# Performance work log

Hardware: AMD Instinct MI355X
Metric: run time of the kernel (lower is better)

Reference implementation:

```python
import jax, jax.numpy as jnp
import numpy as np

H = 32        # attention heads
HKV = 32      # kv heads (MHA)
D = 128       # head size
HID = 4096    # hidden size
B = 4         # sequences in prefill batch
S = 1024      # tokens per sequence
T = B * S     # total tokens
NUM_BLOCKS = 64
BLOCK_SIZE = 128


def setup_inputs() -> dict:
    key = jax.random.key(0)
    ks = jax.random.split(key, 6)
    hidden_states = jax.random.normal(ks[0], (T, HID), jnp.float32) * 0.02
    theta = jax.random.uniform(ks[1], (T, D // 2), jnp.float32) * 6.2831853
    cos = jnp.cos(theta)
    sin = jnp.sin(theta)
    qkv_w = jax.random.normal(ks[2], (HID, (H + 2 * HKV) * D), jnp.float32) * (HID ** -0.5)
    o_w = jax.random.normal(ks[3], (H * D, HID), jnp.float32) * ((H * D) ** -0.5)
    key_cache = jnp.zeros((NUM_BLOCKS, BLOCK_SIZE, HKV, D), jnp.float32)
    value_cache = jnp.zeros((NUM_BLOCKS, BLOCK_SIZE, HKV, D), jnp.float32)
    cu_seqlen_prefill = jnp.arange(B + 1, dtype=jnp.int32) * S
    slots = jnp.arange(T, dtype=jnp.int32)
    block_tables = jnp.arange(B * (S // BLOCK_SIZE), dtype=jnp.int32).reshape(B, S // BLOCK_SIZE)
    input_lengths = jnp.full((B,), S, jnp.int32)
    return dict(hidden_states=hidden_states, cos=cos, sin=sin, qkv_w=qkv_w, o_w=o_w,
                key_cache=key_cache, value_cache=value_cache,
                cu_seqlen_prefill=cu_seqlen_prefill, slots=slots,
                block_tables=block_tables, input_lengths=input_lengths, max_s=S)


def _rope(x, cos, sin):
    # neox-style rotary: split head dim in half. x: [T, h, D], cos/sin: [T, D/2]
    d2 = x.shape[-1] // 2
    x1, x2 = x[..., :d2], x[..., d2:]
    c, s = cos[:, None, :], sin[:, None, :]
    return jnp.concatenate([x1 * c - x2 * s, x2 * c + x1 * s], axis=-1)


def reference(hidden_states, cos, sin, qkv_w, o_w, key_cache, value_cache,
              cu_seqlen_prefill, slots, block_tables, input_lengths, max_s):
    T_ = hidden_states.shape[0]
    B_ = input_lengths.shape[0]
    S_ = T_ // B_  # equal-length prefill sequences per cu_seqlen_prefill
    # fused QKV projection
    qkv = hidden_states @ qkv_w                      # [T, (H+2Hkv)*D]
    q = qkv[:, :H * D].reshape(T_, H, D)
    kv = qkv[:, H * D:].reshape(T_, 2, HKV, D)
    k, v = kv[:, 0], kv[:, 1]
    # rotary embedding on q and k (in-place in original)
    q = _rope(q, cos, sin)
    k = _rope(k, cos, sin)
    # reshape_and_cache: scatter rotated K / raw V into paged KV cache by flat slot
    kc = key_cache.reshape(-1, HKV, D).at[slots].set(k).reshape(key_cache.shape)
    vc = value_cache.reshape(-1, HKV, D).at[slots].set(v).reshape(value_cache.shape)
    # varlen causal flash attention (prefill branch); equal seqlens -> dense [B,S]
    scale = D ** -0.5
    qb = q.reshape(B_, S_, H, D)
    kb = k.reshape(B_, S_, HKV, D)
    vb = v.reshape(B_, S_, HKV, D)
    scores = jnp.einsum('bqhd,bkhd->bhqk', qb, kb) * scale   # [B,H,S,S]
    idx = jnp.arange(S_)
    causal = idx[:, None] >= idx[None, :]
    scores = jnp.where(causal[None, None], scores, jnp.finfo(scores.dtype).min)
    probs = jax.nn.softmax(scores, axis=-1)
    attn = jnp.einsum('bhqk,bkhd->bqhd', probs, vb).reshape(T_, H * D)
    out = attn @ o_w                                 # o_proj, no bias
    return out, kc, vc
```

## Files before the change

kernel.cpp:

```cpp
#include <hip/hip_runtime.h>

#define HQ 32
#define HKV 32
#define DH 128
#define HID 4096
#define BATCH 4
#define SEQ 1024
#define TOK (BATCH * SEQ)
#define NQKV 12288
#define CACHE_ROWS 8192
#define SM_SCALE 0.08838834764831845f

typedef unsigned short u16;
typedef __bf16 bf16x8 __attribute__((ext_vector_type(8)));
typedef float floatx4 __attribute__((ext_vector_type(4)));
typedef u16 u16x8 __attribute__((ext_vector_type(8)));
typedef u16 u16x4 __attribute__((ext_vector_type(4)));

__device__ __forceinline__ u16 f2bf(float x) {
  unsigned u = __float_as_uint(x);
  u += 0x7FFF + ((u >> 16) & 1);
  return (u16)(u >> 16);
}
__device__ __forceinline__ float bf2f(u16 h) {
  return __uint_as_float(((unsigned)h) << 16);
}
__device__ __forceinline__ void cp16(const void* g, void* l) {
  __builtin_amdgcn_global_load_lds(
      (__attribute__((address_space(1))) unsigned int*)(g),
      (__attribute__((address_space(3))) unsigned int*)(l), 16, 0, 0);
}

__global__ void k_f32_to_bf16(const float4* __restrict__ x, ushort4* __restrict__ y) {
  int i = blockIdx.x * 256 + threadIdx.x;
  float4 v = x[i];
  ushort4 o;
  o.x = f2bf(v.x); o.y = f2bf(v.y); o.z = f2bf(v.z); o.w = f2bf(v.w);
  y[i] = o;
}

__global__ void k_transpose_bf16(const float* __restrict__ W, u16* __restrict__ Wt,
                                 int Kd, int Nd) {
  __shared__ float t[64][65];
  int n0 = blockIdx.x << 6, k0 = blockIdx.y << 6;
  int tx = threadIdx.x & 63, ty = threadIdx.x >> 6;
#pragma unroll
  for (int r = ty; r < 64; r += 4)
    t[r][tx] = W[(size_t)(k0 + r) * Nd + n0 + tx];
  __syncthreads();
  const int kg = threadIdx.x & 15, nr = threadIdx.x >> 4;
#pragma unroll
  for (int q = 0; q < 4; ++q) {
    int n = q * 16 + nr;
    u16x4 o;
#pragma unroll
    for (int j = 0; j < 4; ++j) o[j] = f2bf(t[kg * 4 + j][n]);
    *(u16x4*)&Wt[(size_t)(n0 + n) * Kd + k0 + kg * 4] = o;
  }
}

template <int Nd, int Kd, bool OUT_BF16>
__global__ __launch_bounds__(512, 2) void k_gemm256(const u16* __restrict__ A,
                                                    const u16* __restrict__ Bt,
                                                    void* __restrict__ Cp) {
  constexpr int GX = Nd / 256;
  constexpr int NWG = (TOK / 256) * GX;
  constexpr int BAND = 4 * GX;
  __shared__ __align__(16) u16 lds[2][2][256 * 64];

  const int bid = blockIdx.x;
  const int j = (bid & 7) * (NWG / 8) + (bid >> 3);
  const int band = j / BAND, r = j % BAND;
  const int by = band * 4 + (r & 3), bx = r >> 2;
  const int bm = by << 8, bn = bx << 8;

  const int tid = threadIdx.x;
  const int wave = tid >> 6, lane = tid & 63;
  const int wm = wave >> 2, wn = wave & 3;
  const int quad = lane >> 4, l16 = lane & 15;

  auto stage_half = [&](const u16* src, int grow, int k0, u16* ldsb, int h) {
#pragma unroll
    for (int p = 0; p < 2; ++p) {
      int g = tid + (p << 9);
      int row = g >> 3, ps = g & 7;
      int ls = ps ^ (row & 7);
      cp16(src + (size_t)(grow + h * 128 + row) * Kd + k0 + ls * 8,
           ldsb + ((h * 128 + row) << 6) + (ps << 3));
    }
  };
  auto frag = [&](const u16* ldsb, int row, int slot) {
    return (const bf16x8*)(ldsb + (row << 6) + ((slot ^ (row & 7)) << 3));
  };

  const floatx4 FZ4 = {0.f, 0.f, 0.f, 0.f};
  floatx4 acc[8][4];
#pragma unroll
  for (int i = 0; i < 8; ++i)
#pragma unroll
    for (int j2 = 0; j2 < 4; ++j2) acc[i][j2] = FZ4;

  stage_half(A, bm, 0, &lds[0][0][0], 0);
  stage_half(A, bm, 0, &lds[0][0][0], 1);
  stage_half(Bt, bn, 0, &lds[0][1][0], 0);
  stage_half(Bt, bn, 0, &lds[0][1][0], 1);
  stage_half(Bt, bn, 64, &lds[1][1][0], 0);
  stage_half(Bt, bn, 64, &lds[1][1][0], 1);
  asm volatile("s_waitcnt vmcnt(4)" ::: "memory");
  asm volatile("s_barrier" ::: "memory");

  constexpr int NT = Kd / 64;
  for (int t = 0; t < NT; ++t) {
    const int c = t & 1, o = c ^ 1;
    const u16* cA = &lds[c][0][0];
    const u16* cB = &lds[c][1][0];
    const int k1 = (t + 1 < NT) ? (t + 1) * 64 : (Kd - 64);
    const int k2 = (t + 2 < NT) ? (t + 2) * 64 : (Kd - 64);

    bf16x8 bfr[4][2];
#pragma unroll
    for (int ph = 0; ph < 4; ++ph) {
      if (ph == 0) {
#pragma unroll
        for (int ni = 0; ni < 4; ++ni)
#pragma unroll
          for (int ks = 0; ks < 2; ++ks)
            bfr[ni][ks] = *frag(cB, wn * 64 + ni * 16 + l16, ks * 4 + quad);
      }
      bf16x8 af[2][2];
#pragma unroll
      for (int m = 0; m < 2; ++m)
#pragma unroll
        for (int ks = 0; ks < 2; ++ks)
          af[m][ks] = *frag(cA, wm * 128 + (ph * 2 + m) * 16 + l16, ks * 4 + quad);

      if (ph == 0) stage_half(A, bm, k1, &lds[o][0][0], 0);
      else if (ph == 1) stage_half(A, bm, k1, &lds[o][0][0], 1);
      else if (ph == 2) stage_half(Bt, bn, k2, &lds[c][1][0], 0);
      else stage_half(Bt, bn, k2, &lds[c][1][0], 1);

      asm volatile("s_barrier" ::: "memory");
      __builtin_amdgcn_s_setprio(1);
#pragma unroll
      for (int m = 0; m < 2; ++m)
#pragma unroll
        for (int ni = 0; ni < 4; ++ni)
#pragma unroll
          for (int ks = 0; ks < 2; ++ks)
            acc[ph * 2 + m][ni] = __builtin_amdgcn_mfma_f32_16x16x32_bf16(
                af[m][ks], bfr[ni][ks], acc[ph * 2 + m][ni], 0, 0, 0);
      __builtin_amdgcn_s_setprio(0);
      if (ph == 3) asm volatile("s_waitcnt vmcnt(4)" ::: "memory");
      asm volatile("s_barrier" ::: "memory");
    }
  }
  asm volatile("s_waitcnt vmcnt(0)" ::: "memory");

  const int rbase = bm + wm * 128 + quad * 4;
  const int cbase = bn + wn * 64 + l16;
#pragma unroll
  for (int mi = 0; mi < 8; ++mi)
#pragma unroll
    for (int ni = 0; ni < 4; ++ni)
#pragma unroll
      for (int r2 = 0; r2 < 4; ++r2) {
        size_t idx = (size_t)(rbase + mi * 16 + r2) * Nd + (cbase + ni * 16);
        if (OUT_BF16)
          ((u16*)Cp)[idx] = f2bf(acc[mi][ni][r2]);
        else
          ((float*)Cp)[idx] = acc[mi][ni][r2];
      }
}

__global__ void k_rope_scatter(const u16* __restrict__ qkv, const float* __restrict__ cosp,
                               const float* __restrict__ sinp, const int* __restrict__ slots,
                               u16* __restrict__ qb, u16* __restrict__ kb,
                               float* __restrict__ kc, float* __restrict__ vc) {
  const int t = blockIdx.x;
  const int b = t >> 10, s = t & 1023;
  const int tid = threadIdx.x;
  __shared__ float lc[64], ls[64];
  if (tid < 64) lc[tid] = cosp[t * 64 + tid];
  else if (tid < 128) ls[tid - 64] = sinp[t * 64 + (tid - 64)];
  __syncthreads();
  const int slot = slots[t];
  const u16* base = qkv + (size_t)t * NQKV;
  const int h = tid >> 3, i0 = (tid & 7) << 3;
  float c[8], sn[8];
#pragma unroll
  for (int j = 0; j < 8; ++j) { c[j] = lc[i0 + j]; sn[j] = ls[i0 + j]; }

  {
    u16x8 x1 = *(const u16x8*)&base[h * 128 + i0];
    u16x8 x2 = *(const u16x8*)&base[h * 128 + 64 + i0];
    u16x8 y1, y2;
#pragma unroll
    for (int j = 0; j < 8; ++j) {
      float a = bf2f(x1[j]), d = bf2f(x2[j]);
      y1[j] = f2bf((a * c[j] - d * sn[j]) * SM_SCALE);
      y2[j] = f2bf((d * c[j] + a * sn[j]) * SM_SCALE);
    }
    size_t o = ((size_t)(b * HQ + h) * SEQ + s) * DH + i0;
    *(u16x8*)&qb[o] = y1;
    *(u16x8*)&qb[o + 64] = y2;
  }
  {
    u16x8 x1 = *(const u16x8*)&base[HQ * DH + h * 128 + i0];
    u16x8 x2 = *(const u16x8*)&base[HQ * DH + h * 128 + 64 + i0];
    u16x8 y1, y2;
    float f1[8], f2[8];
#pragma unroll
    for (int j = 0; j < 8; ++j) {
      float a = bf2f(x1[j]), d = bf2f(x2[j]);
      f1[j] = a * c[j] - d * sn[j];
      f2[j] = d * c[j] + a * sn[j];
      y1[j] = f2bf(f1[j]);
      y2[j] = f2bf(f2[j]);
    }
    size_t o = ((size_t)(b * HKV + h) * SEQ + s) * DH + i0;
    *(u16x8*)&kb[o] = y1;
    *(u16x8*)&kb[o + 64] = y2;
    size_t oc = (size_t)slot * (HKV * DH) + h * 128 + i0;
    *(float4*)&kc[oc]      = make_float4(f1[0], f1[1], f1[2], f1[3]);
    *(float4*)&kc[oc + 4]  = make_float4(f1[4], f1[5], f1[6], f1[7]);
    *(float4*)&kc[oc + 64] = make_float4(f2[0], f2[1], f2[2], f2[3]);
    *(float4*)&kc[oc + 68] = make_float4(f2[4], f2[5], f2[6], f2[7]);
  }
  {
    const int vo = tid * 16;
    u16x8 va = *(const u16x8*)&base[2 * HQ * DH + vo];
    u16x8 vb2 = *(const u16x8*)&base[2 * HQ * DH + vo + 8];
    float* vd = vc + (size_t)slot * (HKV * DH) + vo;
    *(float4*)&vd[0]  = make_float4(bf2f(va[0]), bf2f(va[1]), bf2f(va[2]), bf2f(va[3]));
    *(float4*)&vd[4]  = make_float4(bf2f(va[4]), bf2f(va[5]), bf2f(va[6]), bf2f(va[7]));
    *(float4*)&vd[8]  = make_float4(bf2f(vb2[0]), bf2f(vb2[1]), bf2f(vb2[2]), bf2f(vb2[3]));
    *(float4*)&vd[12] = make_float4(bf2f(vb2[4]), bf2f(vb2[5]), bf2f(vb2[6]), bf2f(vb2[7]));
  }
}

__global__ void k_vt(const u16* __restrict__ qkv, u16* __restrict__ vT) {
  __shared__ u16 t[64][66];
  const int bh = blockIdx.z;
  const int b = bh >> 5, h = bh & 31;
  const int s0 = blockIdx.y << 6, d0 = blockIdx.x << 6;
  const int cg = threadIdx.x & 15, rr = threadIdx.x >> 4;
#pragma unroll
  for (int q = 0; q < 4; ++q) {
    int r = q * 16 + rr;
    u16x4 v = *(const u16x4*)&qkv[(size_t)(b * SEQ + s0 + r) * NQKV + 2 * HQ * DH +
                                  h * DH + d0 + cg * 4];
    *(u16x4*)&t[r][cg * 4] = v;
  }
  __syncthreads();
#pragma unroll
  for (int q = 0; q < 4; ++q) {
    int d = q * 16 + rr;
    u16x4 o;
#pragma unroll
    for (int j = 0; j < 4; ++j) o[j] = t[cg * 4 + j][d];
    *(u16x4*)&vT[((size_t)bh * DH + d0 + d) * SEQ + s0 + cg * 4] = o;
  }
}

__global__ __launch_bounds__(512, 4) void k_attn(const u16* __restrict__ qb,
                                                 const u16* __restrict__ kb,
                                                 const u16* __restrict__ vT,
                                                 u16* __restrict__ attn) {
  __shared__ __align__(16) u16 lK[2][64 * 128];
  __shared__ __align__(16) u16 lV[2][128 * 64];
  __shared__ __align__(16) u16 lP[128 * 64];
  const int qt = blockIdx.x, h = blockIdx.y, b = blockIdx.z;
  const int bh = b * HQ + h;
  const int q0 = qt << 7;
  const int tid = threadIdx.x, wave = tid >> 6, lane = tid & 63;
  const int quad = lane >> 4, l16 = lane & 15;
  const u16* Qb = qb + (size_t)bh * SEQ * DH;
  const u16* Kb = kb + (size_t)bh * SEQ * DH;
  const u16* Vb = vT + (size_t)bh * DH * SEQ;

  bf16x8 qf[4];
#pragma unroll
  for (int ds = 0; ds < 4; ++ds)
    qf[ds] = *(const bf16x8*)&Qb[(size_t)(q0 + wave * 16 + l16) * DH + ds * 32 + quad * 8];

  const floatx4 FZ4 = {0.f, 0.f, 0.f, 0.f};
  floatx4 acc_o[8];
#pragma unroll
  for (int i = 0; i < 8; ++i) acc_o[i] = FZ4;
  float m_i[4] = {-1e30f, -1e30f, -1e30f, -1e30f};
  float l_i[4] = {0.f, 0.f, 0.f, 0.f};

  auto stageK = [&](int buf, int k0) {
#pragma unroll
    for (int p = 0; p < 2; ++p) {
      int g = tid + (p << 9);
      int row = g >> 4, gs = g & 15;
      int sl = gs ^ (row & 15);
      cp16(Kb + (size_t)(k0 + row) * DH + sl * 8, &lK[buf][g * 8]);
    }
  };
  auto stageV = [&](int buf, int k0) {
#pragma unroll
    for (int p = 0; p < 2; ++p) {
      int g = tid + (p << 9);
      int row = g >> 3, gs = g & 7;
      int sl = gs ^ (row & 7);
      cp16(Vb + (size_t)row * SEQ + k0 + sl * 8, &lV[buf][g * 8]);
    }
  };

  const int ktmax = 2 * qt + 1;
  stageK(0, 0);
  stageV(0, 0);
  for (int kt = 0; kt <= ktmax; ++kt) {
    const int cur = kt & 1;
    const int k0 = kt << 6;
    if (kt < ktmax) {
      stageK(cur ^ 1, k0 + 64);
      stageV(cur ^ 1, k0 + 64);
      asm volatile("s_waitcnt vmcnt(4)" ::: "memory");
    } else {
      asm volatile("s_waitcnt vmcnt(0)" ::: "memory");
    }
    __builtin_amdgcn_s_barrier();

    floatx4 accs[4];
    __builtin_amdgcn_s_setprio(1);
#pragma unroll
    for (int ni = 0; ni < 4; ++ni) {
      accs[ni] = FZ4;
      const int row = ni * 16 + l16;
#pragma unroll
      for (int ds = 0; ds < 4; ++ds) {
        bf16x8 kf = *(const bf16x8*)&lK[cur][row * 128 + (((ds * 4 + quad) ^ (row & 15)) << 3)];
        accs[ni] = __builtin_amdgcn_mfma_f32_16x16x32_bf16(qf[ds], kf, accs[ni], 0, 0, 0);
      }
    }
    __builtin_amdgcn_s_setprio(0);
    if (k0 + 63 > q0 + wave * 16) {
#pragma unroll
      for (int ni = 0; ni < 4; ++ni) {
        int ki = k0 + ni * 16 + l16;
#pragma unroll
        for (int r = 0; r < 4; ++r) {
          int qr = q0 + wave * 16 + quad * 4 + r;
          if (ki > qr) accs[ni][r] = -1e30f;
        }
      }
    }
    float mnew[4], alpha[4];
#pragma unroll
    for (int r = 0; r < 4; ++r) {
      float mx = fmaxf(fmaxf(accs[0][r], accs[1][r]), fmaxf(accs[2][r], accs[3][r]));
#pragma unroll
      for (int off = 1; off < 16; off <<= 1) mx = fmaxf(mx, __shfl_xor(mx, off));
      mnew[r] = fmaxf(m_i[r], mx);
      alpha[r] = __expf(m_i[r] - mnew[r]);
      m_i[r] = mnew[r];
    }
    float rs[4] = {0.f, 0.f, 0.f, 0.f};
#pragma unroll
    for (int ni = 0; ni < 4; ++ni)
#pragma unroll
      for (int r = 0; r < 4; ++r) {
        float p = __expf(accs[ni][r] - mnew[r]);
        rs[r] += p;
        int prow = wave * 16 + quad * 4 + r, pcol = ni * 16 + l16;
        lP[prow * 64 + ((((pcol >> 3) ^ (prow & 7))) << 3) + (pcol & 7)] = f2bf(p);
      }
#pragma unroll
    for (int r = 0; r < 4; ++r) {
      float sr = rs[r];
#pragma unroll
      for (int off = 1; off < 16; off <<= 1) sr += __shfl_xor(sr, off);
      l_i[r] = l_i[r] * alpha[r] + sr;
    }
#pragma unroll
    for (int dt = 0; dt < 8; ++dt)
#pragma unroll
      for (int r = 0; r < 4; ++r) acc_o[dt][r] *= alpha[r];

    bf16x8 pf[2];
    const int prow = wave * 16 + l16;
#pragma unroll
    for (int ks = 0; ks < 2; ++ks)
      pf[ks] = *(const bf16x8*)&lP[prow * 64 + (((ks * 4 + quad) ^ (prow & 7)) << 3)];
    __builtin_amdgcn_s_setprio(1);
#pragma unroll
    for (int dt = 0; dt < 8; ++dt) {
      const int vrow = dt * 16 + l16;
#pragma unroll
      for (int ks = 0; ks < 2; ++ks) {
        bf16x8 vf = *(const bf16x8*)&lV[cur][vrow * 64 + (((ks * 4 + quad) ^ (vrow & 7)) << 3)];
        acc_o[dt] = __builtin_amdgcn_mfma_f32_16x16x32_bf16(pf[ks], vf, acc_o[dt], 0, 0, 0);
      }
    }
    __builtin_amdgcn_s_setprio(0);
    asm volatile("s_waitcnt lgkmcnt(0)" ::: "memory");
    __builtin_amdgcn_s_barrier();
  }
  float inv[4];
#pragma unroll
  for (int r = 0; r < 4; ++r) inv[r] = 1.0f / l_i[r];
#pragma unroll
  for (int dt = 0; dt < 8; ++dt)
#pragma unroll
    for (int r = 0; r < 4; ++r) {
      int tok = b * SEQ + q0 + wave * 16 + quad * 4 + r;
      attn[(size_t)tok * HID + h * DH + dt * 16 + l16] = f2bf(acc_o[dt][r] * inv[r]);
    }
}

extern "C" void kernel_launch(void* const* d_in, const int* in_sizes, int n_in,
                              void* d_out, int out_size, void* d_ws, size_t ws_size,
                              hipStream_t stream) {
  (void)in_sizes; (void)n_in; (void)out_size; (void)ws_size;
  const float* hs = (const float*)d_in[0];
  const float* cosp = (const float*)d_in[1];
  const float* sinp = (const float*)d_in[2];
  const float* qkv_w = (const float*)d_in[3];
  const float* o_w = (const float*)d_in[4];
  const int* slots = (const int*)d_in[8];

  float* out = (float*)d_out;
  float* kc = out + (size_t)TOK * HID;
  float* vc = kc + (size_t)CACHE_ROWS * HKV * DH;

  u16* regA = (u16*)d_ws;
  u16* regB = regA + (size_t)NQKV * HID;
  u16* regC = regB + (size_t)TOK * NQKV;
  u16* W1t = regA;
  u16* qb = regA;
  u16* kb = qb + (size_t)BATCH * HQ * SEQ * DH;
  u16* vTp = kb + (size_t)BATCH * HKV * SEQ * DH;
  u16* qkv = regB;
  u16* W2t = regB;
  u16* hsb = regC;
  u16* attnb = regC;

  const size_t halfRows = (size_t)(CACHE_ROWS - TOK) * HKV * DH;
  hipMemsetAsync(kc + (size_t)TOK * HKV * DH, 0, halfRows * sizeof(float), stream);
  hipMemsetAsync(vc + (size_t)TOK * HKV * DH, 0, halfRows * sizeof(float), stream);

  k_f32_to_bf16<<<TOK * HID / 1024, 256, 0, stream>>>((const float4*)hs, (ushort4*)hsb);
  k_transpose_bf16<<<dim3(NQKV / 64, HID / 64), 256, 0, stream>>>(qkv_w, W1t, HID, NQKV);
  k_gemm256<NQKV, HID, true>
      <<<(TOK / 256) * (NQKV / 256), 512, 0, stream>>>(hsb, W1t, qkv);
  k_rope_scatter<<<TOK, 256, 0, stream>>>(qkv, cosp, sinp, slots, qb, kb, kc, vc);
  k_vt<<<dim3(DH / 64, SEQ / 64, BATCH * HKV), 256, 0, stream>>>(qkv, vTp);
  k_transpose_bf16<<<dim3(HID / 64, HID / 64), 256, 0, stream>>>(o_w, W2t, HID, HID);
  k_attn<<<dim3(SEQ / 128, HQ, BATCH), 512, 0, stream>>>(qb, kb, vTp, attnb);
  k_gemm256<HID, HID, false>
      <<<(TOK / 256) * (HID / 256), 512, 0, stream>>>(attnb, W2t, out);
}
```

Baseline: 1.278 ms.

## Fuse RoPE, KV-cache scatter and V transpose into QKV GEMM epilogue

The QKV GEMM epilogue now stages the bf16 tile in swizzled LDS and applies rotary embedding directly. It writes Q/K in head-major layout, the K/V fp32 caches, and transposed V. This removes the intermediate qkv buffer round trip and two separate kernel launches (rope_scatter and vt). The attention kernel's launch bounds also change from 4 to 2 waves per EU. The epilogue is heavier and the V cache writes use scalar fp32 stores, which may be less coalesced.

```diff
diff --git a/kernel.cpp b/kernel.cpp
--- a/kernel.cpp
+++ b/kernel.cpp
@@ -59,10 +59,12 @@
   }
 }
 
-template <int Nd, int Kd, bool OUT_BF16>
-__global__ __launch_bounds__(512, 2) void k_gemm256(const u16* __restrict__ A,
-                                                    const u16* __restrict__ Bt,
-                                                    void* __restrict__ Cp) {
+template <int Nd, int Kd, int MODE>
+__global__ __launch_bounds__(512, 2) void k_gemm256(
+    const u16* __restrict__ A, const u16* __restrict__ Bt, void* __restrict__ Cp,
+    const float* __restrict__ cosp, const float* __restrict__ sinp,
+    const int* __restrict__ slots, u16* __restrict__ qbp, u16* __restrict__ kbp,
+    float* __restrict__ kcp, float* __restrict__ vcp, u16* __restrict__ vTp) {
   constexpr int GX = Nd / 256;
   constexpr int NWG = (TOK / 256) * GX;
   constexpr int BAND = 4 * GX;
@@ -155,114 +157,126 @@
     }
   }
   asm volatile("s_waitcnt vmcnt(0)" ::: "memory");
-
-  const int rbase = bm + wm * 128 + quad * 4;
-  const int cbase = bn + wn * 64 + l16;
+  __syncthreads();
+
+  if (MODE == 0) {
+    const int rbase = bm + wm * 128 + quad * 4;
+    const int cbase = bn + wn * 64 + l16;
+#pragma unroll
+    for (int mi = 0; mi < 8; ++mi)
+#pragma unroll
+      for (int ni = 0; ni < 4; ++ni)
+#pragma unroll
+        for (int r2 = 0; r2 < 4; ++r2) {
+          size_t idx = (size_t)(rbase + mi * 16 + r2) * Nd + (cbase + ni * 16);
+          ((float*)Cp)[idx] = acc[mi][ni][r2];
+        }
+    return;
+  }
+
+  u16* Ct = (u16*)&lds[0][0][0];
 #pragma unroll
   for (int mi = 0; mi < 8; ++mi)
 #pragma unroll
-    for (int ni = 0; ni < 4; ++ni)
+    for (int r2 = 0; r2 < 4; ++r2) {
+      int row = wm * 128 + mi * 16 + quad * 4 + r2;
+      int sw8 = (row ^ (row >> 3)) & 7;
+#pragma unroll
+      for (int ni = 0; ni < 4; ++ni) {
+        int col = wn * 64 + ni * 16 + l16;
+        Ct[row * 256 + (((col >> 3) ^ sw8) << 3) + (col & 7)] = f2bf(acc[mi][ni][r2]);
+      }
+    }
+  const bool isV = (bn >= 2 * HQ * DH);
+  if (isV) {
+    const int chb = bn - 2 * HQ * DH + wn * 64 + l16;
+#pragma unroll
+    for (int mi = 0; mi < 8; ++mi)
 #pragma unroll
       for (int r2 = 0; r2 < 4; ++r2) {
-        size_t idx = (size_t)(rbase + mi * 16 + r2) * Nd + (cbase + ni * 16);
-        if (OUT_BF16)
-          ((u16*)Cp)[idx] = f2bf(acc[mi][ni][r2]);
-        else
-          ((float*)Cp)[idx] = acc[mi][ni][r2];
-      }
-}
-
-__global__ void k_rope_scatter(const u16* __restrict__ qkv, const float* __restrict__ cosp,
-                               const float* __restrict__ sinp, const int* __restrict__ slots,
-                               u16* __restrict__ qb, u16* __restrict__ kb,
-                               float* __restrict__ kc, float* __restrict__ vc) {
-  const int t = blockIdx.x;
-  const int b = t >> 10, s = t & 1023;
-  const int tid = threadIdx.x;
-  __shared__ float lc[64], ls[64];
-  if (tid < 64) lc[tid] = cosp[t * 64 + tid];
-  else if (tid < 128) ls[tid - 64] = sinp[t * 64 + (tid - 64)];
+        int t = bm + wm * 128 + mi * 16 + quad * 4 + r2;
+        int slot = slots[t];
+#pragma unroll
+        for (int ni = 0; ni < 4; ++ni)
+          vcp[(size_t)slot * (HKV * DH) + chb + ni * 16] = acc[mi][ni][r2];
+      }
+  }
   __syncthreads();
-  const int slot = slots[t];
-  const u16* base = qkv + (size_t)t * NQKV;
-  const int h = tid >> 3, i0 = (tid & 7) << 3;
-  float c[8], sn[8];
-#pragma unroll
-  for (int j = 0; j < 8; ++j) { c[j] = lc[i0 + j]; sn[j] = ls[i0 + j]; }
-
-  {
-    u16x8 x1 = *(const u16x8*)&base[h * 128 + i0];
-    u16x8 x2 = *(const u16x8*)&base[h * 128 + 64 + i0];
-    u16x8 y1, y2;
-#pragma unroll
-    for (int j = 0; j < 8; ++j) {
-      float a = bf2f(x1[j]), d = bf2f(x2[j]);
-      y1[j] = f2bf((a * c[j] - d * sn[j]) * SM_SCALE);
-      y2[j] = f2bf((d * c[j] + a * sn[j]) * SM_SCALE);
-    }
-    size_t o = ((size_t)(b * HQ + h) * SEQ + s) * DH + i0;
-    *(u16x8*)&qb[o] = y1;
-    *(u16x8*)&qb[o + 64] = y2;
-  }
-  {
-    u16x8 x1 = *(const u16x8*)&base[HQ * DH + h * 128 + i0];
-    u16x8 x2 = *(const u16x8*)&base[HQ * DH + h * 128 + 64 + i0];
-    u16x8 y1, y2;
-    float f1[8], f2[8];
-#pragma unroll
-    for (int j = 0; j < 8; ++j) {
-      float a = bf2f(x1[j]), d = bf2f(x2[j]);
-      f1[j] = a * c[j] - d * sn[j];
-      f2[j] = d * c[j] + a * sn[j];
-      y1[j] = f2bf(f1[j]);
-      y2[j] = f2bf(f2[j]);
-    }
-    size_t o = ((size_t)(b * HKV + h) * SEQ + s) * DH + i0;
-    *(u16x8*)&kb[o] = y1;
-    *(u16x8*)&kb[o + 64] = y2;
-    size_t oc = (size_t)slot * (HKV * DH) + h * 128 + i0;
-    *(float4*)&kc[oc]      = make_float4(f1[0], f1[1], f1[2], f1[3]);
-    *(float4*)&kc[oc + 4]  = make_float4(f1[4], f1[5], f1[6], f1[7]);
-    *(float4*)&kc[oc + 64] = make_float4(f2[0], f2[1], f2[2], f2[3]);
-    *(float4*)&kc[oc + 68] = make_float4(f2[4], f2[5], f2[6], f2[7]);
-  }
-  {
-    const int vo = tid * 16;
-    u16x8 va = *(const u16x8*)&base[2 * HQ * DH + vo];
-    u16x8 vb2 = *(const u16x8*)&base[2 * HQ * DH + vo + 8];
-    float* vd = vc + (size_t)slot * (HKV * DH) + vo;
-    *(float4*)&vd[0]  = make_float4(bf2f(va[0]), bf2f(va[1]), bf2f(va[2]), bf2f(va[3]));
-    *(float4*)&vd[4]  = make_float4(bf2f(va[4]), bf2f(va[5]), bf2f(va[6]), bf2f(va[7]));
-    *(float4*)&vd[8]  = make_float4(bf2f(vb2[0]), bf2f(vb2[1]), bf2f(vb2[2]), bf2f(vb2[3]));
-    *(float4*)&vd[12] = make_float4(bf2f(vb2[4]), bf2f(vb2[5]), bf2f(vb2[6]), bf2f(vb2[7]));
-  }
-}
-
-__global__ void k_vt(const u16* __restrict__ qkv, u16* __restrict__ vT) {
-  __shared__ u16 t[64][66];
-  const int bh = blockIdx.z;
-  const int b = bh >> 5, h = bh & 31;
-  const int s0 = blockIdx.y << 6, d0 = blockIdx.x << 6;
-  const int cg = threadIdx.x & 15, rr = threadIdx.x >> 4;
-#pragma unroll
-  for (int q = 0; q < 4; ++q) {
-    int r = q * 16 + rr;
-    u16x4 v = *(const u16x4*)&qkv[(size_t)(b * SEQ + s0 + r) * NQKV + 2 * HQ * DH +
-                                  h * DH + d0 + cg * 4];
-    *(u16x4*)&t[r][cg * 4] = v;
-  }
-  __syncthreads();
-#pragma unroll
-  for (int q = 0; q < 4; ++q) {
-    int d = q * 16 + rr;
-    u16x4 o;
-#pragma unroll
-    for (int j = 0; j < 4; ++j) o[j] = t[cg * 4 + j][d];
-    *(u16x4*)&vT[((size_t)bh * DH + d0 + d) * SEQ + s0 + cg * 4] = o;
-  }
-}
-
-__global__ __launch_bounds__(512, 4) void k_attn(const u16* __restrict__ qb,
+
+  if (!isV) {
+    const bool isQ = (bn < HQ * DH);
+    const int hbase = isQ ? (bn >> 7) : ((bn - HQ * DH) >> 7);
+#pragma unroll
+    for (int it = 0; it < 8; ++it) {
+      int u = tid + (it << 9);
+      int tk = u >> 4, hh = (u >> 3) & 1, grp = u & 7;
+      int t = bm + tk, bb = t >> 10, ss = t & 1023;
+      int sw8 = (tk ^ (tk >> 3)) & 7;
+      int c1 = hh * 128 + grp * 8;
+      u16x8 x1 = *(const u16x8*)&Ct[tk * 256 + (((c1 >> 3) ^ sw8) << 3)];
+      u16x8 x2 = *(const u16x8*)&Ct[tk * 256 + ((((c1 + 64) >> 3) ^ sw8) << 3)];
+      float4 c0 = *(const float4*)&cosp[t * 64 + grp * 8];
+      float4 c4 = *(const float4*)&cosp[t * 64 + grp * 8 + 4];
+      float4 s0 = *(const float4*)&sinp[t * 64 + grp * 8];
+      float4 s4 = *(const float4*)&sinp[t * 64 + grp * 8 + 4];
+      float cc[8] = {c0.x, c0.y, c0.z, c0.w, c4.x, c4.y, c4.z, c4.w};
+      float sn[8] = {s0.x, s0.y, s0.z, s0.w, s4.x, s4.y, s4.z, s4.w};
+      float f1[8], f2[8];
+      u16x8 y1, y2;
+#pragma unroll
+      for (int jj = 0; jj < 8; ++jj) {
+        float a = bf2f(x1[jj]), d = bf2f(x2[jj]);
+        f1[jj] = a * cc[jj] - d * sn[jj];
+        f2[jj] = d * cc[jj] + a * sn[jj];
+      }
+      if (isQ) {
+#pragma unroll
+        for (int jj = 0; jj < 8; ++jj) {
+          y1[jj] = f2bf(f1[jj] * SM_SCALE);
+          y2[jj] = f2bf(f2[jj] * SM_SCALE);
+        }
+        size_t oq = ((size_t)(bb * HQ + hbase + hh) * SEQ + ss) * DH + grp * 8;
+        *(u16x8*)&qbp[oq] = y1;
+        *(u16x8*)&qbp[oq + 64] = y2;
+      } else {
+#pragma unroll
+        for (int jj = 0; jj < 8; ++jj) {
+          y1[jj] = f2bf(f1[jj]);
+          y2[jj] = f2bf(f2[jj]);
+        }
+        size_t ok = ((size_t)(bb * HKV + hbase + hh) * SEQ + ss) * DH + grp * 8;
+        *(u16x8*)&kbp[ok] = y1;
+        *(u16x8*)&kbp[ok + 64] = y2;
+        int slot = slots[t];
+        size_t oc = (size_t)slot * (HKV * DH) + (hbase + hh) * 128 + grp * 8;
+        *(float4*)&kcp[oc] = make_float4(f1[0], f1[1], f1[2], f1[3]);
+        *(float4*)&kcp[oc + 4] = make_float4(f1[4], f1[5], f1[6], f1[7]);
+        *(float4*)&kcp[oc + 64] = make_float4(f2[0], f2[1], f2[2], f2[3]);
+        *(float4*)&kcp[oc + 68] = make_float4(f2[4], f2[5], f2[6], f2[7]);
+      }
+    }
+  } else {
+    const int hvb = (bn - 2 * HQ * DH) >> 7;
+#pragma unroll
+    for (int it = 0; it < 16; ++it) {
+      int u = tid + (it << 9);
+      int sgrp = u & 31, dd = (u >> 5) & 127, hh = u >> 12;
+      int col = hh * 128 + dd, cg = col >> 3, ce = col & 7;
+      u16x8 o;
+#pragma unroll
+      for (int jj = 0; jj < 8; ++jj) {
+        int row = sgrp * 8 + jj;
+        int sw8 = (row ^ (row >> 3)) & 7;
+        o[jj] = Ct[row * 256 + ((cg ^ sw8) << 3) + ce];
+      }
+      int t0 = bm + sgrp * 8;
+      int bb = t0 >> 10, ss = t0 & 1023;
+      *(u16x8*)&vTp[((size_t)(bb * HKV + hvb + hh) * DH + dd) * SEQ + ss] = o;
+    }
+  }
+}
+
+__global__ __launch_bounds__(512, 2) void k_attn(const u16* __restrict__ qb,
                                                  const u16* __restrict__ kb,
                                                  const u16* __restrict__ vT,
                                                  u16* __restrict__ attn) {
@@ -428,13 +442,12 @@
 
   u16* regA = (u16*)d_ws;
   u16* regB = regA + (size_t)NQKV * HID;
-  u16* regC = regB + (size_t)TOK * NQKV;
+  u16* regC = regB + (size_t)NQKV * HID;
   u16* W1t = regA;
-  u16* qb = regA;
+  u16* W2t = regA;
+  u16* qb = regB;
   u16* kb = qb + (size_t)BATCH * HQ * SEQ * DH;
   u16* vTp = kb + (size_t)BATCH * HKV * SEQ * DH;
-  u16* qkv = regB;
-  u16* W2t = regB;
   u16* hsb = regC;
   u16* attnb = regC;
 
@@ -444,12 +457,11 @@
 
   k_f32_to_bf16<<<TOK * HID / 1024, 256, 0, stream>>>((const float4*)hs, (ushort4*)hsb);
   k_transpose_bf16<<<dim3(NQKV / 64, HID / 64), 256, 0, stream>>>(qkv_w, W1t, HID, NQKV);
-  k_gemm256<NQKV, HID, true>
-      <<<(TOK / 256) * (NQKV / 256), 512, 0, stream>>>(hsb, W1t, qkv);
-  k_rope_scatter<<<TOK, 256, 0, stream>>>(qkv, cosp, sinp, slots, qb, kb, kc, vc);
-  k_vt<<<dim3(DH / 64, SEQ / 64, BATCH * HKV), 256, 0, stream>>>(qkv, vTp);
+  k_gemm256<NQKV, HID, 1><<<(TOK / 256) * (NQKV / 256), 512, 0, stream>>>(
+      hsb, W1t, nullptr, cosp, sinp, slots, qb, kb, kc, vc, vTp);
   k_transpose_bf16<<<dim3(HID / 64, HID / 64), 256, 0, stream>>>(o_w, W2t, HID, HID);
   k_attn<<<dim3(SEQ / 128, HQ, BATCH), 512, 0, stream>>>(qb, kb, vTp, attnb);
-  k_gemm256<HID, HID, false>
-      <<<(TOK / 256) * (HID / 256), 512, 0, stream>>>(attnb, W2t, out);
-}
+  k_gemm256<HID, HID, 0><<<(TOK / 256) * (HID / 256), 512, 0, stream>>>(
+      attnb, W2t, out, nullptr, nullptr, nullptr, nullptr, nullptr, nullptr, nullptr,
+      nullptr);
+}
```

Result: no change. 1.279 ms (+0.1%).
